# Kernel tuning notes

Measured on AMD Instinct MI355X. Metric: run time of the kernel, lower is better.

The kernel has to match this reference:

```python
import jax, jax.numpy as jnp
import numpy as np

BATCH = 1048576
INPUT_DIM = 64
DEPTH = 7
N_INTERNAL = 2 ** DEPTH - 1  # 127
N_LEAVES = 2 ** DEPTH        # 128


def setup_inputs() -> dict:
    key = jax.random.key(0)
    kx, kw = jax.random.split(key)
    x = jax.random.normal(kx, (BATCH, INPUT_DIM), dtype=jnp.float32)
    node_weights = jax.random.normal(kw, (N_INTERNAL, INPUT_DIM), dtype=jnp.float32) * 0.01
    node_biases = jnp.zeros((N_INTERNAL,), dtype=jnp.float32)
    leaf_values = jnp.linspace(0.0, 1.0, N_LEAVES, dtype=jnp.float32)
    return {"x": x, "node_weights": node_weights, "node_biases": node_biases,
            "leaf_values": leaf_values}


def _leaf_probs(x, node_weights, node_biases, depth):
    # All node routing probabilities in one GEMM (BFS node order matches idx order).
    logits = jnp.einsum('bd,nd->bn', x, node_weights) + node_biases  # [B, n_internal]
    p_right = jax.nn.sigmoid(logits)
    batch = x.shape[0]
    probs = jnp.ones((batch, 1), dtype=x.dtype)  # root prob
    idx = 0
    for d in range(depth):
        n = 1 << d
        pd = p_right[:, idx:idx + n]  # [B, n] nodes at level d in BFS order
        # child order: left (2*node) then right (2*node+1) -> interleave
        probs = jnp.stack([probs * (1.0 - pd), probs * pd], axis=-1).reshape(batch, 2 * n)
        idx += n
    return probs  # [B, n_leaves]


def reference(x, node_weights, node_biases, leaf_values):
    leaf_probs = _leaf_probs(x, node_weights, node_biases, DEPTH)
    pred = leaf_probs @ leaf_values  # [B]
    return (pred, leaf_probs)
```

## Files before the change

kernel.cpp:

```cpp
#include <hip/hip_runtime.h>


typedef float v4f __attribute__((ext_vector_type(4)));
typedef _Float16 h8 __attribute__((ext_vector_type(8)));
typedef unsigned int u32;
typedef u32 u32x2 __attribute__((ext_vector_type(2)));

constexpr int BATCH = 1 << 20;
constexpr int PSTRIDE = 40;
constexpr int PWAVE = 128 * PSTRIDE;

__device__ __forceinline__ float fast_sigmoid(float z) {
    float e = __builtin_amdgcn_exp2f(z * -1.44269504088896340736f);
    return __builtin_amdgcn_rcpf(1.0f + e);
}

__global__ __launch_bounds__(256) void sdt_kernel(
    const float* __restrict__ x,
    const float* __restrict__ w,
    const float* __restrict__ bias,
    const float* __restrict__ leaf,
    float* __restrict__ pred_out,
    float* __restrict__ lp_out)
{
    __shared__ __align__(16) unsigned char smem[4 * PWAVE];

    const int tid  = threadIdx.x;
    const int lane = tid & 63;
    const int wave = tid >> 6;
    const int lc = lane & 15, lq = lane >> 4;
    const int j = lane & 7,   rsub = lane >> 3;

    unsigned char* Pw = smem + wave * PWAVE;

    h8 bfrag[8][2];
#pragma unroll
    for (int ct = 0; ct < 8; ++ct) {
        int node = ct * 16 + lc; if (node > 126) node = 126;
#pragma unroll
        for (int kh = 0; kh < 2; ++kh) {
            const float* src = w + node * 64 + kh * 32 + lq * 8;
            v4f f0 = *(const v4f*)src;
            v4f f1 = *(const v4f*)(src + 4);
            h8 b;
#pragma unroll
            for (int t = 0; t < 4; ++t) { b[t] = (_Float16)f0[t]; b[4 + t] = (_Float16)f1[t]; }
            bfrag[ct][kh] = b;
        }
    }
    float bias_v[8];
#pragma unroll
    for (int ct = 0; ct < 8; ++ct) {
        int node = ct * 16 + lc; if (node > 126) node = 126;
        bias_v[ct] = bias[node];
    }
    v4f leafv[4];
#pragma unroll
    for (int s = 0; s < 4; ++s) leafv[s] = *(const v4f*)(leaf + 32 * s + 4 * j);

    const int b2 = (j >> 2) & 1, b3 = (j >> 1) & 1, b4 = j & 1;

    for (int ck = 0; ck < 4; ++ck) {
        const int row0 = blockIdx.x * 256 + ck * 64 + wave * 16;

        const float* xr = x + (size_t)(row0 + lc) * 64 + lq * 8;
        v4f xa = *(const v4f*)xr,        xb = *(const v4f*)(xr + 4);
        v4f xc = *(const v4f*)(xr + 32), xd = *(const v4f*)(xr + 36);
        h8 a0, a1;
#pragma unroll
        for (int t = 0; t < 4; ++t) {
            a0[t] = (_Float16)xa[t]; a0[4 + t] = (_Float16)xb[t];
            a1[t] = (_Float16)xc[t]; a1[4 + t] = (_Float16)xd[t];
        }

#pragma unroll
        for (int ct = 0; ct < 8; ++ct) {
            v4f acc = {};
            acc = __builtin_amdgcn_mfma_f32_16x16x32_f16(a0, bfrag[ct][0], acc, 0, 0, 0);
            acc = __builtin_amdgcn_mfma_f32_16x16x32_f16(a1, bfrag[ct][1], acc, 0, 0, 0);
            union { _Float16 h[4]; u32x2 wrd; } u;
#pragma unroll
            for (int i = 0; i < 4; ++i)
                u.h[i] = (_Float16)fast_sigmoid(acc[i] + bias_v[ct]);
            *(u32x2*)(Pw + (ct * 16 + lc) * PSTRIDE + lq * 8) = u.wrd;
        }

        asm volatile("s_waitcnt lgkmcnt(0)" ::: "memory");

        auto rd = [&](int node, int row) -> float {
            return (float)*(const _Float16*)(Pw + node * PSTRIDE + row * 2);
        };

        float pa = 0.f, pb = 0.f;
#pragma unroll
        for (int i1 = 0; i1 < 2; ++i1) {
            const int row = rsub + 8 * i1;
            float p0  = rd(0, row);
            float p1a = rd(1, row), p1b = rd(2, row);
            float f01_0 = (1.f - p0) * (1.f - p1a);
            float f01_1 = (1.f - p0) * p1a;
            float f01_2 = p0 * (1.f - p1b);
            float f01_3 = p0 * p1b;
            float acc = 0.f;
            v4f* dst = (v4f*)lp_out + (size_t)(row0 + row) * 32 + j;
#pragma unroll
            for (int seg = 0; seg < 4; ++seg) {
                float f01 = seg == 0 ? f01_0 : seg == 1 ? f01_1 : seg == 2 ? f01_2 : f01_3;
                float pd2 = rd(3 + seg, row);
                float P3 = f01 * (b2 ? pd2 : 1.f - pd2);
                float pd3 = rd(7 + 2 * seg + (j >> 2), row);
                float P4 = P3 * (b3 ? pd3 : 1.f - pd3);
                float pd4 = rd(15 + 4 * seg + (j >> 1), row);
                float P5 = P4 * (b4 ? pd4 : 1.f - pd4);
                const int q = 8 * seg + j;
                float pd5 = rd(31 + q, row);
                float A = P5 * (1.f - pd5), B = P5 * pd5;
                float pl = rd(63 + 2 * q, row), pr = rd(64 + 2 * q, row);
                v4f o = { A * (1.f - pl), A * pl, B * (1.f - pr), B * pr };
                __builtin_nontemporal_store(o, dst + seg * 8);
                acc = fmaf(o.x, leafv[seg].x, acc);
                acc = fmaf(o.y, leafv[seg].y, acc);
                acc = fmaf(o.z, leafv[seg].z, acc);
                acc = fmaf(o.w, leafv[seg].w, acc);
            }
            if (i1 == 0) pa = acc; else pb = acc;
        }

#pragma unroll
        for (int s = 1; s <= 4; s <<= 1) {
            pa += __shfl_xor(pa, s, 64);
            pb += __shfl_xor(pb, s, 64);
        }
        if (j == 0) {
            pred_out[row0 + rsub]     = pa;
            pred_out[row0 + rsub + 8] = pb;
        }
    }
}

extern "C" void kernel_launch(void* const* d_in, const int* in_sizes, int n_in,
                              void* d_out, int out_size, void* d_ws, size_t ws_size,
                              hipStream_t stream) {
    const float* x    = (const float*)d_in[0];
    const float* w    = (const float*)d_in[1];
    const float* bias = (const float*)d_in[2];
    const float* leaf = (const float*)d_in[3];

    float* pred = (float*)d_out;
    float* lp   = (float*)d_out + BATCH;

    sdt_kernel<<<BATCH / 256, 256, 0, stream>>>(x, w, bias, leaf, pred, lp);
}
```

Baseline: 183.4 us.

## Prefetch next chunk of x, use packed f16 conversions, and set occupancy hint

Loads the x rows for the next 64-row chunk while the current chunk runs its MFMA, sigmoid and leaf-product work, so global load latency overlaps compute. Float-to-half conversions now use packed cvt_pkrtz instructions instead of per-element casts, which cuts VALU instruction count. The launch bounds now request three blocks per CU and the chunk loop is fully unrolled. The prefetch holds extra registers live, and round-toward-zero conversion changes rounding slightly.

New measurement: 177.5 us. 3.2% less time.

```diff
diff --git a/kernel.cpp b/kernel.cpp
--- a/kernel.cpp
+++ b/kernel.cpp
@@ -15,7 +15,20 @@
     return __builtin_amdgcn_rcpf(1.0f + e);
 }
 
-__global__ __launch_bounds__(256) void sdt_kernel(
+__device__ __forceinline__ u32 pk2(float a, float b) {
+    return __builtin_bit_cast(u32, __builtin_amdgcn_cvt_pkrtz(a, b));
+}
+
+__device__ __forceinline__ h8 cvt8(v4f lo, v4f hi) {
+    union { u32 w[4]; h8 v; } u;
+    u.w[0] = pk2(lo.x, lo.y);
+    u.w[1] = pk2(lo.z, lo.w);
+    u.w[2] = pk2(hi.x, hi.y);
+    u.w[3] = pk2(hi.z, hi.w);
+    return u.v;
+}
+
+__global__ __launch_bounds__(256, 3) void sdt_kernel(
     const float* __restrict__ x,
     const float* __restrict__ w,
     const float* __restrict__ bias,
@@ -40,12 +53,7 @@
 #pragma unroll
         for (int kh = 0; kh < 2; ++kh) {
             const float* src = w + node * 64 + kh * 32 + lq * 8;
-            v4f f0 = *(const v4f*)src;
-            v4f f1 = *(const v4f*)(src + 4);
-            h8 b;
-#pragma unroll
-            for (int t = 0; t < 4; ++t) { b[t] = (_Float16)f0[t]; b[4 + t] = (_Float16)f1[t]; }
-            bfrag[ct][kh] = b;
+            bfrag[ct][kh] = cvt8(*(const v4f*)src, *(const v4f*)(src + 4));
         }
     }
     float bias_v[8];
@@ -59,18 +67,22 @@
     for (int s = 0; s < 4; ++s) leafv[s] = *(const v4f*)(leaf + 32 * s + 4 * j);
 
     const int b2 = (j >> 2) & 1, b3 = (j >> 1) & 1, b4 = j & 1;
+    const int wave_row0 = blockIdx.x * 256 + wave * 16;
 
+    const float* xr0 = x + (size_t)(wave_row0 + lc) * 64 + lq * 8;
+    v4f xa = *(const v4f*)xr0,        xb = *(const v4f*)(xr0 + 4);
+    v4f xc = *(const v4f*)(xr0 + 32), xd = *(const v4f*)(xr0 + 36);
+
+#pragma unroll
     for (int ck = 0; ck < 4; ++ck) {
-        const int row0 = blockIdx.x * 256 + ck * 64 + wave * 16;
+        const int row0 = wave_row0 + ck * 64;
 
-        const float* xr = x + (size_t)(row0 + lc) * 64 + lq * 8;
-        v4f xa = *(const v4f*)xr,        xb = *(const v4f*)(xr + 4);
-        v4f xc = *(const v4f*)(xr + 32), xd = *(const v4f*)(xr + 36);
-        h8 a0, a1;
-#pragma unroll
-        for (int t = 0; t < 4; ++t) {
-            a0[t] = (_Float16)xa[t]; a0[4 + t] = (_Float16)xb[t];
-            a1[t] = (_Float16)xc[t]; a1[4 + t] = (_Float16)xd[t];
+        h8 a0 = cvt8(xa, xb);
+        h8 a1 = cvt8(xc, xd);
+        if (ck < 3) {
+            const float* xr = xr0 + (ck + 1) * 64 * 64;
+            xa = *(const v4f*)xr;        xb = *(const v4f*)(xr + 4);
+            xc = *(const v4f*)(xr + 32); xd = *(const v4f*)(xr + 36);
         }
 
 #pragma unroll
@@ -78,11 +90,12 @@
             v4f acc = {};
             acc = __builtin_amdgcn_mfma_f32_16x16x32_f16(a0, bfrag[ct][0], acc, 0, 0, 0);
             acc = __builtin_amdgcn_mfma_f32_16x16x32_f16(a1, bfrag[ct][1], acc, 0, 0, 0);
-            union { _Float16 h[4]; u32x2 wrd; } u;
-#pragma unroll
-            for (int i = 0; i < 4; ++i)
-                u.h[i] = (_Float16)fast_sigmoid(acc[i] + bias_v[ct]);
-            *(u32x2*)(Pw + (ct * 16 + lc) * PSTRIDE + lq * 8) = u.wrd;
+            float s0 = fast_sigmoid(acc[0] + bias_v[ct]);
+            float s1 = fast_sigmoid(acc[1] + bias_v[ct]);
+            float s2 = fast_sigmoid(acc[2] + bias_v[ct]);
+            float s3 = fast_sigmoid(acc[3] + bias_v[ct]);
+            *(u32x2*)(Pw + (ct * 16 + lc) * PSTRIDE + lq * 8) =
+                u32x2{pk2(s0, s1), pk2(s2, s3)};
         }
 
         asm volatile("s_waitcnt lgkmcnt(0)" ::: "memory");
```
